# Performance work log

Hardware: AMD Instinct MI355X
Metric: run time of the kernel (lower is better)

The kernel has to match this reference:

```python
import jax, jax.numpy as jnp
import numpy as np

EMBED_PHI = 1024
EMBED_F = 1024
HIDDEN_F = 1024
N_HEADS = 16
B, S = 2, 2048


def setup_inputs() -> dict:
    key = jax.random.key(0)
    ks = jax.random.split(key, 9)
    sphi = 1.0 / np.sqrt(EMBED_PHI)
    sf = 1.0 / np.sqrt(EMBED_F)
    sh = 1.0 / np.sqrt(HIDDEN_F)
    return {
        "q": jax.random.normal(ks[0], (B, S, EMBED_PHI), jnp.float32),
        "k": jax.random.normal(ks[1], (B, S, EMBED_PHI), jnp.float32),
        "v": jax.random.normal(ks[2], (B, S, EMBED_F), jnp.float32),
        "Wq": jax.random.normal(ks[3], (HIDDEN_F, EMBED_PHI), jnp.float32) * sphi,
        "Wk": jax.random.normal(ks[4], (HIDDEN_F, EMBED_PHI), jnp.float32) * sphi,
        "Wv": jax.random.normal(ks[5], (HIDDEN_F, EMBED_F), jnp.float32) * sf,
        "bv": jax.random.normal(ks[6], (HIDDEN_F,), jnp.float32) * sf,
        "Wo": jax.random.normal(ks[7], (EMBED_F, HIDDEN_F), jnp.float32) * sh,
        "bo": jax.random.normal(ks[8], (EMBED_F,), jnp.float32) * sh,
    }


def reference(q, k, v, Wq, Wk, Wv, bv, Wo, bo):
    Bq, Sq, _ = q.shape
    hd = HIDDEN_F // N_HEADS
    scale = 1.0 / np.sqrt(hd)
    # projections; torch Linear: y = x @ W.T + b
    qh = (q @ Wq.T).reshape(Bq, Sq, N_HEADS, hd).transpose(0, 2, 1, 3)  # [B,H,S,d]
    kh = (k @ Wk.T).reshape(Bq, Sq, N_HEADS, hd).transpose(0, 2, 1, 3)
    vh = (v @ Wv.T + bv).reshape(Bq, Sq, N_HEADS, hd).transpose(0, 2, 1, 3)
    scores = jnp.einsum("bhsd,bhtd->bhst", qh, kh) * scale  # [B,H,S,S]
    # mask: triu(diagonal=0) masked (attend strictly to past) except [0,0] unmasked
    mask = jnp.triu(jnp.ones((Sq, Sq), dtype=bool), k=0).at[0, 0].set(False)
    scores = jnp.where(mask, -jnp.inf, scores)
    probs = jax.nn.softmax(scores, axis=-1)  # dropout is identity at eval
    out = jnp.einsum("bhst,bhtd->bhsd", probs, vh)
    out = out.transpose(0, 2, 1, 3).reshape(Bq, Sq, HIDDEN_F)
    return out @ Wo.T + bo
```

## Files before the change

kernel.cpp:

```cpp
#include <hip/hip_runtime.h>
#include <hip/hip_bf16.h>

typedef __attribute__((ext_vector_type(8))) short short8;
typedef __attribute__((ext_vector_type(4))) float f32x4;

#define NE  1024
#define SEQ 2048

__device__ __forceinline__ float bf2f(unsigned short u) {
    union { unsigned u; float f; } x; x.u = ((unsigned)u) << 16; return x.f;
}
__device__ __forceinline__ unsigned short f2bf(float f) {
    union { float f; unsigned u; } x; x.f = f;
    unsigned r = x.u + 0x7FFFu + ((x.u >> 16) & 1u);
    return (unsigned short)(r >> 16);
}
__device__ __forceinline__ unsigned short f2bf_fast(float f) {
    union { float f; unsigned u; } x; x.f = f;
    return (unsigned short)((x.u + 0x8000u) >> 16);
}

__global__ void detect_dtype(const unsigned short* __restrict__ s,
                             int* __restrict__ flag) {
    __shared__ int cnt;
    const int t = threadIdx.x;
    if (t == 0) cnt = 0;
    __syncthreads();
    unsigned short u = s[t];
    int e = (u >> 7) & 0xFF;
    int sane = (e == 0) || (e >= 100 && e <= 140);
    atomicAdd(&cnt, sane);
    __syncthreads();
    if (t == 0) flag[0] = (cnt >= 230) ? 1 : 0;
}

struct Ptrs7 { const void* s[7]; unsigned short* d[7]; };

__global__ void convert7(Ptrs7 p, const int* __restrict__ flag, int zoff) {
    const int z = blockIdx.z + zoff;
    const int n = (z < 3) ? (4 << 20) : (1 << 20);
    const bool in_f32 = (flag[0] == 0);
    unsigned short* d = p.d[z];
    const int stride = gridDim.x * blockDim.x;
    for (int i8 = blockIdx.x * blockDim.x + threadIdx.x; i8 * 8 < n; i8 += stride) {
        size_t off = (size_t)i8 * 8;
        if (in_f32) {
            const float* sp = (const float*)p.s[z] + off;
            float4 a = *(const float4*)sp, b2 = *(const float4*)(sp + 4);
            short8 sv;
            sv[0] = (short)f2bf(a.x);  sv[1] = (short)f2bf(a.y);
            sv[2] = (short)f2bf(a.z);  sv[3] = (short)f2bf(a.w);
            sv[4] = (short)f2bf(b2.x); sv[5] = (short)f2bf(b2.y);
            sv[6] = (short)f2bf(b2.z); sv[7] = (short)f2bf(b2.w);
            *(short8*)(d + off) = sv;
        } else {
            *(short8*)(d + off) = *(const short8*)((const unsigned short*)p.s[z] + off);
        }
    }
}

template<int AWS, int WWS, int OUTF>
__global__ __launch_bounds__(256, 3)
void gemm_bt(const void* A0, const void* A1, const void* A2,
             const void* W0, const void* W1, const void* W2,
             const void* b0, const void* b1, const void* b2,
             void* C0, void* C1, void* C2,
             const int* __restrict__ flag)
{
    __shared__ __align__(16) unsigned short As[128 * 32];
    __shared__ __align__(16) unsigned short Bs[128 * 32];
    const int z = blockIdx.z;
    const void* Ap = (z == 0) ? A0 : (z == 1) ? A1 : A2;
    const void* Wp = (z == 0) ? W0 : (z == 1) ? W1 : W2;
    const void* bp = (z == 0) ? b0 : (z == 1) ? b1 : b2;
    void*       Cp = (z == 0) ? C0 : (z == 1) ? C1 : C2;
    const bool in_f32 = (flag[0] == 0);
    const int t = threadIdx.x;
    const int w = t >> 6, l = t & 63, q = l >> 4, n = l & 15;
    const int m0 = blockIdx.y * 128, n0 = blockIdx.x * 128;
    const int wm = (w >> 1) * 64, wn = (w & 1) * 64;
    const int srow = t >> 2, sk = (t & 3) * 8;

    f32x4 acc[4][4] = {};

    for (int k0 = 0; k0 < NE; k0 += 32) {
        if (AWS || !in_f32) {
            #pragma unroll
            for (int hh = 0; hh < 2; hh++) {
                const unsigned short* ga = (const unsigned short*)Ap +
                    (size_t)(m0 + srow + hh * 64) * NE + k0 + sk;
                __builtin_amdgcn_global_load_lds(
                    (const __attribute__((address_space(1))) void*)ga,
                    (__attribute__((address_space(3))) void*)&As[hh * 2048 + w * 512],
                    16, 0, 0);
            }
        } else {
            #pragma unroll
            for (int hh = 0; hh < 2; hh++) {
                const float* a = (const float*)Ap +
                                 (size_t)(m0 + srow + hh * 64) * NE + k0 + sk;
                float4 x0 = *(const float4*)a, x1 = *(const float4*)(a + 4);
                short8 sv;
                sv[0] = (short)f2bf(x0.x); sv[1] = (short)f2bf(x0.y);
                sv[2] = (short)f2bf(x0.z); sv[3] = (short)f2bf(x0.w);
                sv[4] = (short)f2bf(x1.x); sv[5] = (short)f2bf(x1.y);
                sv[6] = (short)f2bf(x1.z); sv[7] = (short)f2bf(x1.w);
                *(short8*)(&As[hh * 2048 + t * 8]) = sv;
            }
        }
        if (WWS || !in_f32) {
            #pragma unroll
            for (int hh = 0; hh < 2; hh++) {
                const unsigned short* ga = (const unsigned short*)Wp +
                    (size_t)(n0 + srow + hh * 64) * NE + k0 + sk;
                __builtin_amdgcn_global_load_lds(
                    (const __attribute__((address_space(1))) void*)ga,
                    (__attribute__((address_space(3))) void*)&Bs[hh * 2048 + w * 512],
                    16, 0, 0);
            }
        } else {
            #pragma unroll
            for (int hh = 0; hh < 2; hh++) {
                const float* a = (const float*)Wp +
                                 (size_t)(n0 + srow + hh * 64) * NE + k0 + sk;
                float4 x0 = *(const float4*)a, x1 = *(const float4*)(a + 4);
                short8 sv;
                sv[0] = (short)f2bf(x0.x); sv[1] = (short)f2bf(x0.y);
                sv[2] = (short)f2bf(x0.z); sv[3] = (short)f2bf(x0.w);
                sv[4] = (short)f2bf(x1.x); sv[5] = (short)f2bf(x1.y);
                sv[6] = (short)f2bf(x1.z); sv[7] = (short)f2bf(x1.w);
                *(short8*)(&Bs[hh * 2048 + t * 8]) = sv;
            }
        }
        __syncthreads();

        short8 af[4], bfv[4];
        #pragma unroll
        for (int mt = 0; mt < 4; mt++)
            af[mt] = *(const short8*)(&As[(wm + mt * 16 + n) * 32 + q * 8]);
        #pragma unroll
        for (int nt = 0; nt < 4; nt++)
            bfv[nt] = *(const short8*)(&Bs[(wn + nt * 16 + n) * 32 + q * 8]);
        #pragma unroll
        for (int mt = 0; mt < 4; mt++)
            #pragma unroll
            for (int nt = 0; nt < 4; nt++)
                acc[mt][nt] = __builtin_amdgcn_mfma_f32_16x16x32_bf16(
                    af[mt], bfv[nt], acc[mt][nt], 0, 0, 0);
        __syncthreads();
    }

    #pragma unroll
    for (int mt = 0; mt < 4; mt++)
        #pragma unroll
        for (int nt = 0; nt < 4; nt++)
            #pragma unroll
            for (int r = 0; r < 4; r++) {
                int row = m0 + wm + mt * 16 + q * 4 + r;
                int col = n0 + wn + nt * 16 + n;
                float v2 = acc[mt][nt][r];
                if (bp)
                    v2 += in_f32 ? ((const float*)bp)[col]
                                 : bf2f(((const unsigned short*)bp)[col]);
                size_t idx = (size_t)row * NE + col;
                if (OUTF && in_f32) ((float*)Cp)[idx] = v2;
                else                ((unsigned short*)Cp)[idx] = f2bf(v2);
            }
}

__global__ __launch_bounds__(512, 4)
void attn(const unsigned short* qh, const unsigned short* kh,
          const unsigned short* vh, unsigned short* ctx)
{
    __shared__ __align__(16) unsigned short Ks[64 * 72];
    __shared__ __align__(16) unsigned short Vt[64 * 72];
    __shared__ __align__(16) unsigned short Ps[8][16 * 72];
    const int t = threadIdx.x, w = t >> 6, l = t & 63;
    const int q = l >> 4, n = l & 15;
    const int half = w >> 2, sub = w & 3;
    const int pair = blockIdx.x;
    const int qbB = pair, qbA = 31 - pair;
    const int qb = half ? qbB : qbA;
    const int h = blockIdx.y, b = blockIdx.z;
    const size_t base = (size_t)b * SEQ * NE + h * 64;
    const int i0 = qb * 64 + sub * 16;

    short8 qf[2];
    qf[0] = *(const short8*)(&qh[base + (size_t)(i0 + n) * NE + q * 8]);
    qf[1] = *(const short8*)(&qh[base + (size_t)(i0 + n) * NE + 32 + q * 8]);

    f32x4 o[4] = {};
    float ls[4] = {0.f, 0.f, 0.f, 0.f};

    const float K1 = 0.125f * 1.4426950408889634f;
    const float B2 = 24.0f * 1.4426950408889634f;

    const int kr = t >> 3, kc = (t & 7) * 8;
    const int j2 = (t & 31) * 2, d8 = ((t >> 5) & 7) * 8;

    short8 pk, pv0, pv1;
    pk = *(const short8*)(&kh[base + (size_t)kr * NE + kc]);
    if (t < 256) {
        pv0 = *(const short8*)(&vh[base + (size_t)j2 * NE + d8]);
        pv1 = *(const short8*)(&vh[base + (size_t)(j2 + 1) * NE + d8]);
    }

    unsigned short* PsW = &Ps[w][0];

    for (int jt = 0; jt <= qbA; jt++) {
        *(short8*)(&Ks[kr * 72 + kc]) = pk;
        if (t < 256) {
            #pragma unroll
            for (int e = 0; e < 8; e++) {
                unsigned pkd = (unsigned)(unsigned short)pv0[e] |
                               ((unsigned)(unsigned short)pv1[e] << 16);
                *(unsigned*)(&Vt[(d8 + e) * 72 + j2]) = pkd;
            }
        }
        __syncthreads();

        if (jt < qbA) {
            const int jn = (jt + 1) * 64;
            pk = *(const short8*)(&kh[base + (size_t)(jn + kr) * NE + kc]);
            if (t < 256) {
                pv0 = *(const short8*)(&vh[base + (size_t)(jn + j2) * NE + d8]);
                pv1 = *(const short8*)(&vh[base + (size_t)(jn + j2 + 1) * NE + d8]);
            }
        }

        if (jt <= qb) {
            f32x4 sa[4] = {};
            #pragma unroll
            for (int ks = 0; ks < 2; ks++)
                #pragma unroll
                for (int nt = 0; nt < 4; nt++) {
                    short8 kf = *(const short8*)(&Ks[(nt * 16 + n) * 72 + ks * 32 + q * 8]);
                    sa[nt] = __builtin_amdgcn_mfma_f32_16x16x32_bf16(qf[ks], kf, sa[nt], 0, 0, 0);
                }

            const bool diag = (jt == qb);
            #pragma unroll
            for (int nt = 0; nt < 4; nt++)
                #pragma unroll
                for (int r = 0; r < 4; r++) {
                    float e = fmaf(sa[nt][r], K1, -B2);
                    if (diag) {
                        int j = jt * 64 + nt * 16 + n;
                        int i = i0 + q * 4 + r;
                        bool ok = (j < i) || (i == 0 && j == 0);
                        e = ok ? e : -256.0f;
                    }
                    float p = __builtin_amdgcn_exp2f(e);
                    ls[r] += p;
                    PsW[(q * 4 + r) * 72 + nt * 16 + n] = f2bf_fast(p);
                }
            asm volatile("s_waitcnt lgkmcnt(0)" ::: "memory");

            #pragma unroll
            for (int ks = 0; ks < 2; ks++) {
                short8 pf = *(const short8*)(&PsW[n * 72 + ks * 32 + q * 8]);
                #pragma unroll
                for (int dt = 0; dt < 4; dt++) {
                    short8 vf = *(const short8*)(&Vt[(dt * 16 + n) * 72 + ks * 32 + q * 8]);
                    o[dt] = __builtin_amdgcn_mfma_f32_16x16x32_bf16(pf, vf, o[dt], 0, 0, 0);
                }
            }
        }
        __syncthreads();
    }

    #pragma unroll
    for (int r = 0; r < 4; r++)
        #pragma unroll
        for (int xm = 1; xm <= 8; xm <<= 1)
            ls[r] += __shfl_xor(ls[r], xm, 64);

    #pragma unroll
    for (int r = 0; r < 4; r++) {
        float inv = 1.0f / ls[r];
        #pragma unroll
        for (int dt = 0; dt < 4; dt++)
            ctx[base + (size_t)(i0 + q * 4 + r) * NE + dt * 16 + n] =
                f2bf(o[dt][r] * inv);
    }
}

extern "C" void kernel_launch(void* const* d_in, const int* in_sizes, int n_in,
                              void* d_out, int out_size, void* d_ws, size_t ws_size,
                              hipStream_t stream) {
    const void* q  = d_in[0];
    const void* k  = d_in[1];
    const void* v  = d_in[2];
    const void* Wq = d_in[3];
    const void* Wk = d_in[4];
    const void* Wv = d_in[5];
    const void* bv = d_in[6];
    const void* Wo = d_in[7];
    const void* bo = d_in[8];

    const size_t MB = 1024 * 1024;
    const size_t M4 = 4 * MB;
    unsigned short* ws = (unsigned short*)d_ws;
    unsigned short* qh  = ws;
    unsigned short* kh  = ws + 1 * M4;
    unsigned short* vh  = ws + 2 * M4;
    unsigned short* ctx = qh;

    int tier = (ws_size >= 56 * MB + 64) ? 2 : (ws_size >= 32 * MB + 64) ? 1 : 0;

    unsigned short *qc, *kc, *vc, *Wqc, *Wkc, *Wvc, *Woc;
    int* flag;
    if (tier == 2) {
        qc = ws + 3 * M4; kc = ws + 4 * M4; vc = ws + 5 * M4;
        Wqc = ws + 6 * M4;           Wkc = Wqc + 1 * MB;
        Wvc = Wqc + 2 * MB;          Woc = Wqc + 3 * MB;
        flag = (int*)((char*)d_ws + 56 * MB);
    } else if (tier == 1) {
        qc = kc = vc = nullptr;
        Wqc = ws + 3 * M4;           Wkc = Wqc + 1 * MB;
        Wvc = Wqc + 2 * MB;          Woc = Wqc + 3 * MB;
        flag = (int*)((char*)d_ws + 32 * MB);
    } else {
        qc = kc = vc = nullptr; Wqc = Wkc = Wvc = Woc = nullptr;
        flag = (int*)((char*)d_ws + 24 * MB);
    }

    detect_dtype<<<1, 256, 0, stream>>>((const unsigned short*)q, flag);

    if (tier > 0) {
        Ptrs7 p;
        p.s[0] = q;  p.s[1] = k;  p.s[2] = v;
        p.s[3] = Wq; p.s[4] = Wk; p.s[5] = Wv; p.s[6] = Wo;
        p.d[0] = qc; p.d[1] = kc; p.d[2] = vc;
        p.d[3] = Wqc; p.d[4] = Wkc; p.d[5] = Wvc; p.d[6] = Woc;
        if (tier == 2)
            convert7<<<dim3(512, 1, 7), 256, 0, stream>>>(p, flag, 0);
        else
            convert7<<<dim3(512, 1, 4), 256, 0, stream>>>(p, flag, 3);
    }

    if (tier == 2)
        gemm_bt<1, 1, 0><<<dim3(8, 32, 3), 256, 0, stream>>>(
            qc, kc, vc, Wqc, Wkc, Wvc, nullptr, nullptr, bv, qh, kh, vh, flag);
    else if (tier == 1)
        gemm_bt<0, 1, 0><<<dim3(8, 32, 3), 256, 0, stream>>>(
            q, k, v, Wqc, Wkc, Wvc, nullptr, nullptr, bv, qh, kh, vh, flag);
    else
        gemm_bt<0, 0, 0><<<dim3(8, 32, 3), 256, 0, stream>>>(
            q, k, v, Wq, Wk, Wv, nullptr, nullptr, bv, qh, kh, vh, flag);

    attn<<<dim3(16, 16, 2), 512, 0, stream>>>(qh, kh, vh, ctx);

    if (tier > 0)
        gemm_bt<1, 1, 1><<<dim3(8, 32, 1), 256, 0, stream>>>(
            ctx, ctx, ctx, Woc, Woc, Woc, bo, bo, bo, d_out, d_out, d_out, flag);
    else
        gemm_bt<1, 0, 1><<<dim3(8, 32, 1), 256, 0, stream>>>(
            ctx, ctx, ctx, Wo, Wo, Wo, bo, bo, bo, d_out, d_out, d_out, flag);
}
```

Measured before the change: 242.0 us.

## Write V transposed from projection GEMM and restructure attention with 128-key tiles

The V projection epilogue now writes V in a per-head transposed [B,H,d,S] layout, so attention can copy V tiles straight into LDS with vector stores instead of the scalar transpose scatter. Attention switches from 512-thread blocks handling paired query tiles to 256-thread blocks with one query tile each (reversed order for load balance). Each iteration loads 128 keys, processed as two 64-key halves. The changes aim to cut LDS transpose cost and per-iteration sync overhead. In exchange they drop the causal pairing balance, use more registers for prefetch, and make the GEMM transposed-store pattern strided (4-element chunks).

```diff
diff --git a/kernel.cpp b/kernel.cpp
--- a/kernel.cpp
+++ b/kernel.cpp
@@ -3,6 +3,7 @@
 
 typedef __attribute__((ext_vector_type(8))) short short8;
 typedef __attribute__((ext_vector_type(4))) float f32x4;
+typedef __attribute__((ext_vector_type(4))) unsigned short us4;
 
 #define NE  1024
 #define SEQ 2048
@@ -59,7 +60,7 @@
     }
 }
 
-template<int AWS, int WWS, int OUTF>
+template<int AWS, int WWS, int OUTF, int VT>
 __global__ __launch_bounds__(256, 3)
 void gemm_bt(const void* A0, const void* A1, const void* A2,
              const void* W0, const void* W1, const void* W2,
@@ -153,37 +154,48 @@
     #pragma unroll
     for (int mt = 0; mt < 4; mt++)
         #pragma unroll
-        for (int nt = 0; nt < 4; nt++)
-            #pragma unroll
-            for (int r = 0; r < 4; r++) {
-                int row = m0 + wm + mt * 16 + q * 4 + r;
-                int col = n0 + wn + nt * 16 + n;
-                float v2 = acc[mt][nt][r];
-                if (bp)
-                    v2 += in_f32 ? ((const float*)bp)[col]
-                                 : bf2f(((const unsigned short*)bp)[col]);
-                size_t idx = (size_t)row * NE + col;
-                if (OUTF && in_f32) ((float*)Cp)[idx] = v2;
-                else                ((unsigned short*)Cp)[idx] = f2bf(v2);
-            }
-}
-
-__global__ __launch_bounds__(512, 4)
+        for (int nt = 0; nt < 4; nt++) {
+            int row0 = m0 + wm + mt * 16 + q * 4;
+            int col  = n0 + wn + nt * 16 + n;
+            float bia = 0.f;
+            if (bp)
+                bia = in_f32 ? ((const float*)bp)[col]
+                             : bf2f(((const unsigned short*)bp)[col]);
+            if (VT && z == 2) {
+                int bb = row0 >> 11, s0 = row0 & 2047;
+                int hh2 = col >> 6, dd = col & 63;
+                us4 pk4;
+                #pragma unroll
+                for (int r = 0; r < 4; r++)
+                    pk4[r] = f2bf(acc[mt][nt][r] + bia);
+                *(us4*)((unsigned short*)Cp +
+                        ((size_t)((bb * 16 + hh2) * 64 + dd) << 11) + s0) = pk4;
+            } else {
+                #pragma unroll
+                for (int r = 0; r < 4; r++) {
+                    float v2 = acc[mt][nt][r] + bia;
+                    size_t idx = (size_t)(row0 + r) * NE + col;
+                    if (OUTF && in_f32) ((float*)Cp)[idx] = v2;
+                    else                ((unsigned short*)Cp)[idx] = f2bf(v2);
+                }
+            }
+        }
+}
+
+__global__ __launch_bounds__(256, 3)
 void attn(const unsigned short* qh, const unsigned short* kh,
-          const unsigned short* vh, unsigned short* ctx)
+          const unsigned short* vt, unsigned short* ctx)
 {
-    __shared__ __align__(16) unsigned short Ks[64 * 72];
-    __shared__ __align__(16) unsigned short Vt[64 * 72];
-    __shared__ __align__(16) unsigned short Ps[8][16 * 72];
+    __shared__ __align__(16) unsigned short Ks[128 * 72];
+    __shared__ __align__(16) unsigned short Vt[64 * 136];
+    __shared__ __align__(16) unsigned short Ps[4][16 * 72];
     const int t = threadIdx.x, w = t >> 6, l = t & 63;
     const int q = l >> 4, n = l & 15;
-    const int half = w >> 2, sub = w & 3;
-    const int pair = blockIdx.x;
-    const int qbB = pair, qbA = 31 - pair;
-    const int qb = half ? qbB : qbA;
+    const int qb = 31 - blockIdx.x;
     const int h = blockIdx.y, b = blockIdx.z;
     const size_t base = (size_t)b * SEQ * NE + h * 64;
-    const int i0 = qb * 64 + sub * 16;
+    const size_t vbase = (size_t)((b * 16 + h) * 64) << 11;
+    const int i0 = qb * 64 + w * 16;
 
     short8 qf[2];
     qf[0] = *(const short8*)(&qh[base + (size_t)(i0 + n) * NE + q * 8]);
@@ -195,57 +207,59 @@
     const float K1 = 0.125f * 1.4426950408889634f;
     const float B2 = 24.0f * 1.4426950408889634f;
 
-    const int kr = t >> 3, kc = (t & 7) * 8;
-    const int j2 = (t & 31) * 2, d8 = ((t >> 5) & 7) * 8;
-
-    short8 pk, pv0, pv1;
-    pk = *(const short8*)(&kh[base + (size_t)kr * NE + kc]);
-    if (t < 256) {
-        pv0 = *(const short8*)(&vh[base + (size_t)j2 * NE + d8]);
-        pv1 = *(const short8*)(&vh[base + (size_t)(j2 + 1) * NE + d8]);
+    const int jtmax = qb >> 1;
+    short8 pk[4], pv[4];
+    #pragma unroll
+    for (int i = 0; i < 4; i++) {
+        int c = t + i * 256;
+        pk[i] = *(const short8*)(&kh[base + (size_t)(c >> 3) * NE + (c & 7) * 8]);
+        pv[i] = *(const short8*)(&vt[vbase + ((size_t)(c >> 4) << 11) + (c & 15) * 8]);
     }
 
     unsigned short* PsW = &Ps[w][0];
 
-    for (int jt = 0; jt <= qbA; jt++) {
-        *(short8*)(&Ks[kr * 72 + kc]) = pk;
-        if (t < 256) {
-            #pragma unroll
-            for (int e = 0; e < 8; e++) {
-                unsigned pkd = (unsigned)(unsigned short)pv0[e] |
-                               ((unsigned)(unsigned short)pv1[e] << 16);
-                *(unsigned*)(&Vt[(d8 + e) * 72 + j2]) = pkd;
-            }
+    for (int jt = 0; jt <= jtmax; jt++) {
+        #pragma unroll
+        for (int i = 0; i < 4; i++) {
+            int c = t + i * 256;
+            *(short8*)(&Ks[(c >> 3) * 72 + (c & 7) * 8]) = pk[i];
+            *(short8*)(&Vt[(c >> 4) * 136 + (c & 15) * 8]) = pv[i];
         }
         __syncthreads();
 
-        if (jt < qbA) {
-            const int jn = (jt + 1) * 64;
-            pk = *(const short8*)(&kh[base + (size_t)(jn + kr) * NE + kc]);
-            if (t < 256) {
-                pv0 = *(const short8*)(&vh[base + (size_t)(jn + j2) * NE + d8]);
-                pv1 = *(const short8*)(&vh[base + (size_t)(jn + j2 + 1) * NE + d8]);
-            }
-        }
-
-        if (jt <= qb) {
+        if (jt < jtmax) {
+            const int jn = (jt + 1) * 128;
+            #pragma unroll
+            for (int i = 0; i < 4; i++) {
+                int c = t + i * 256;
+                pk[i] = *(const short8*)(&kh[base + (size_t)(jn + (c >> 3)) * NE + (c & 7) * 8]);
+                pv[i] = *(const short8*)(&vt[vbase + ((size_t)(c >> 4) << 11) + jn + (c & 15) * 8]);
+            }
+        }
+
+        #pragma unroll
+        for (int khalf = 0; khalf < 2; khalf++) {
+            const int kstart = jt * 128 + khalf * 64;
+            if (kstart > qb * 64) break;
+            const bool diag = (kstart == qb * 64);
+            const int kloc = khalf * 64;
+
             f32x4 sa[4] = {};
             #pragma unroll
             for (int ks = 0; ks < 2; ks++)
                 #pragma unroll
                 for (int nt = 0; nt < 4; nt++) {
-                    short8 kf = *(const short8*)(&Ks[(nt * 16 + n) * 72 + ks * 32 + q * 8]);
+                    short8 kf = *(const short8*)(&Ks[(kloc + nt * 16 + n) * 72 + ks * 32 + q * 8]);
                     sa[nt] = __builtin_amdgcn_mfma_f32_16x16x32_bf16(qf[ks], kf, sa[nt], 0, 0, 0);
                 }
 
-            const bool diag = (jt == qb);
             #pragma unroll
             for (int nt = 0; nt < 4; nt++)
                 #pragma unroll
                 for (int r = 0; r < 4; r++) {
                     float e = fmaf(sa[nt][r], K1, -B2);
                     if (diag) {
-                        int j = jt * 64 + nt * 16 + n;
+                        int j = kstart + nt * 16 + n;
                         int i = i0 + q * 4 + r;
                         bool ok = (j < i) || (i == 0 && j == 0);
                         e = ok ? e : -256.0f;
@@ -261,10 +275,11 @@
                 short8 pf = *(const short8*)(&PsW[n * 72 + ks * 32 + q * 8]);
                 #pragma unroll
                 for (int dt = 0; dt < 4; dt++) {
-                    short8 vf = *(const short8*)(&Vt[(dt * 16 + n) * 72 + ks * 32 + q * 8]);
+                    short8 vf = *(const short8*)(&Vt[(dt * 16 + n) * 136 + kloc + ks * 32 + q * 8]);
                     o[dt] = __builtin_amdgcn_mfma_f32_16x16x32_bf16(pf, vf, o[dt], 0, 0, 0);
                 }
             }
+            asm volatile("" ::: "memory");
         }
         __syncthreads();
     }
@@ -303,7 +318,7 @@
     unsigned short* ws = (unsigned short*)d_ws;
     unsigned short* qh  = ws;
     unsigned short* kh  = ws + 1 * M4;
-    unsigned short* vh  = ws + 2 * M4;
+    unsigned short* vt  = ws + 2 * M4;
     unsigned short* ctx = qh;
 
     int tier = (ws_size >= 56 * MB + 64) ? 2 : (ws_size >= 32 * MB + 64) ? 1 : 0;
@@ -340,21 +355,21 @@
     }
 
     if (tier == 2)
-        gemm_bt<1, 1, 0><<<dim3(8, 32, 3), 256, 0, stream>>>(
-            qc, kc, vc, Wqc, Wkc, Wvc, nullptr, nullptr, bv, qh, kh, vh, flag);
+        gemm_bt<1, 1, 0, 1><<<dim3(8, 32, 3), 256, 0, stream>>>(
+            qc, kc, vc, Wqc, Wkc, Wvc, nullptr, nullptr, bv, qh, kh, vt, flag);
     else if (tier == 1)
-        gemm_bt<0, 1, 0><<<dim3(8, 32, 3), 256, 0, stream>>>(
-            q, k, v, Wqc, Wkc, Wvc, nullptr, nullptr, bv, qh, kh, vh, flag);
+        gemm_bt<0, 1, 0, 1><<<dim3(8, 32, 3), 256, 0, stream>>>(
+            q, k, v, Wqc, Wkc, Wvc, nullptr, nullptr, bv, qh, kh, vt, flag);
     else
-        gemm_bt<0, 0, 0><<<dim3(8, 32, 3), 256, 0, stream>>>(
-            q, k, v, Wq, Wk, Wv, nullptr, nullptr, bv, qh, kh, vh, flag);
-
-    attn<<<dim3(16, 16, 2), 512, 0, stream>>>(qh, kh, vh, ctx);
+        gemm_bt<0, 0, 0, 1><<<dim3(8, 32, 3), 256, 0, stream>>>(
+            q, k, v, Wq, Wk, Wv, nullptr, nullptr, bv, qh, kh, vt, flag);
+
+    attn<<<dim3(32, 16, 2), 256, 0, stream>>>(qh, kh, vt, ctx);
 
     if (tier > 0)
-        gemm_bt<1, 1, 1><<<dim3(8, 32, 1), 256, 0, stream>>>(
+        gemm_bt<1, 1, 1, 0><<<dim3(8, 32, 1), 256, 0, stream>>>(
             ctx, ctx, ctx, Woc, Woc, Woc, bo, bo, bo, d_out, d_out, d_out, flag);
     else
-        gemm_bt<1, 0, 1><<<dim3(8, 32, 1), 256, 0, stream>>>(
+        gemm_bt<1, 0, 1, 0><<<dim3(8, 32, 1), 256, 0, stream>>>(
             ctx, ctx, ctx, Wo, Wo, Wo, bo, bo, bo, d_out, d_out, d_out, flag);
 }
```

After: 258.0 us. 6.6% more time.
